# Kernel optimization log

Hardware: AMD Instinct MI355X
Metric: run time of the kernel (lower is better)

Reference implementation:

```python
import jax, jax.numpy as jnp
import numpy as np

B, S, H, L, O = 128, 2048, 128, 2, 2  # batch, seq, hidden(=input), layers, output


def setup_inputs() -> dict:
    key = jax.random.key(0)
    k1, k2, k3, k4, k5 = jax.random.split(key, 5)
    std = 1.0 / np.sqrt(H)
    x_data = jax.random.normal(k1, (B, S, H), dtype=jnp.float32)
    x_length = jax.random.randint(k2, (B,), 0, S, dtype=jnp.int32)
    x_label = jax.random.uniform(k3, (B,), dtype=jnp.float32)
    # torch Linear layout: y = x @ W.T ; init uniform(-1/sqrt(H), 1/sqrt(H))
    Wx2h = jax.random.uniform(k4, (L, 2 * H, H), minval=-std, maxval=std, dtype=jnp.float32)
    Wfc = jax.random.uniform(k5, (L, O, H), minval=-std, maxval=std, dtype=jnp.float32)
    return {"x_data": x_data, "x_length": x_length, "x_label": x_label,
            "Wx2h": Wx2h, "Wfc": Wfc}


def reference(x_data, x_length, x_label, Wx2h, Wfc):
    Bn, Sn, Hn = x_data.shape
    Ln = Wx2h.shape[0]
    # valid-timestep mask: seq index < x_length[i]
    mask = (jnp.arange(Sn)[None, :] < x_length[:, None]).astype(x_data.dtype)  # [B,S]

    def step(carry, inp):
        S1, S2 = carry            # each [L,B,H]
        x_t, m_t = inp            # [B,H], [B]
        h = x_t
        out = None
        S1_new, S2_new = [], []
        for l in range(Ln):
            gate = h @ Wx2h[l].T                    # [B,2H]
            m1, m2 = jnp.split(gate, 2, axis=1)
            s1n = S1[l] + jnp.tanh(m1)
            s2n = S2[l] + jnp.tanh(m2)
            Fu = jax.nn.relu(s1n)
            h = (1.0 - Fu) * s2n + Fu * S2[l]       # hy
            out = jax.nn.softmax(h @ Wfc[l].T, axis=1)  # [B,O]
            S1_new.append(s1n)
            S2_new.append(s2n)
        loss_t = m_t * (x_label - jax.nn.sigmoid(out[:, 1])) ** 2  # [B]
        return (jnp.stack(S1_new), jnp.stack(S2_new)), loss_t

    S0 = jnp.zeros((Ln, Bn, Hn), x_data.dtype)
    xs = (jnp.swapaxes(x_data, 0, 1), mask.T)  # time-major [S,B,H], [S,B]
    _, losses = jax.lax.scan(step, (S0, S0), xs)
    return jnp.sum(losses)
```

## Files before the change

### kernel.cpp

```cpp
#include <hip/hip_runtime.h>

typedef __bf16 bf16;
typedef __bf16 bf16x8 __attribute__((ext_vector_type(8)));
typedef float floatx4 __attribute__((ext_vector_type(4)));

#define BATCH 128
#define SEQ   2048
#define HID   128
#define TWOH  256
#define CH    128
#define NCH   16
#define MTOT  (BATCH * SEQ)

__device__ __forceinline__ float fast_tanh(float x) {
    float e = __builtin_amdgcn_exp2f(2.88539008177793f * x);
    return 1.0f - 2.0f * __builtin_amdgcn_rcpf(e + 1.0f);
}
__device__ __forceinline__ float fast_sigmoid(float x) {
    return __builtin_amdgcn_rcpf(1.0f + __builtin_amdgcn_exp2f(-1.44269504088896f * x));
}

union PK4 { unsigned long long u; bf16 h[4]; };
union PK8 { uint4 u; bf16 h[8]; };

__global__ __launch_bounds__(256) void convert_w_k(const float* __restrict__ W,
                                                   bf16* __restrict__ Wb) {
    int i = blockIdx.x * 256 + threadIdx.x;
    float4 v = ((const float4*)W)[i];
    PK4 pk;
    pk.h[0] = (bf16)v.x; pk.h[1] = (bf16)v.y;
    pk.h[2] = (bf16)v.z; pk.h[3] = (bf16)v.w;
    ((unsigned long long*)Wb)[i] = pk.u;
}

__device__ __forceinline__ void tile_prefix(const float g[4][4], float pref[4][4],
                                            float* stripe_tot, int quad, int l16) {
    float mibase = 0.f;
    #pragma unroll
    for (int mi = 0; mi < 4; ++mi) {
        float s0 = g[mi][0];
        float s1 = s0 + g[mi][1];
        float s2 = s1 + g[mi][2];
        float s3 = s2 + g[mi][3];
        float tot = s3, xq = tot;
        float t = __shfl_up(xq, 16);
        if (quad >= 1) xq += t;
        t = __shfl_up(xq, 32);
        if (quad >= 2) xq += t;
        float excl = mibase + xq - tot;
        pref[mi][0] = excl + s0;
        pref[mi][1] = excl + s1;
        pref[mi][2] = excl + s2;
        pref[mi][3] = excl + s3;
        mibase += __shfl(xq, 48 + l16);
    }
    *stripe_tot = mibase;
}

__device__ __forceinline__ void load_wf(const bf16* __restrict__ Wh, bf16x8 wf[4][2],
                                        int wc, int quad, int l16) {
    #pragma unroll
    for (int s = 0; s < 4; ++s)
        #pragma unroll
        for (int ni = 0; ni < 2; ++ni) {
            int n = wc * 32 + ni * 16 + l16;
            int kg = s * 4 + quad;
            wf[s][ni] = *(const bf16x8*)&Wh[n * 128 + kg * 8];
        }
}

__device__ __forceinline__ void gemm_tile(const bf16* As, const bf16x8 wf[4][2],
                                          floatx4 acc[4][2], int wr, int quad, int l16) {
    #pragma unroll
    for (int s = 0; s < 4; ++s) {
        int kg = s * 4 + quad;
        bf16x8 af[4];
        #pragma unroll
        for (int mi = 0; mi < 4; ++mi) {
            int r = wr * 64 + mi * 16 + l16;
            af[mi] = *(const bf16x8*)&As[r * 128 + ((kg ^ (r & 7)) << 3)];
        }
        #pragma unroll
        for (int mi = 0; mi < 4; ++mi)
            #pragma unroll
            for (int ni = 0; ni < 2; ++ni)
                acc[mi][ni] = __builtin_amdgcn_mfma_f32_16x16x32_bf16(
                    af[mi], wf[s][ni], acc[mi][ni], 0, 0, 0);
    }
}


__global__ __launch_bounds__(512, 4) void l0_k(const float* __restrict__ x,
                                               const bf16* __restrict__ Wb,
                                               uint4* __restrict__ T,
                                               float* __restrict__ Pout) {
    __shared__ bf16 As[128 * 128];
    __shared__ float psum[512];

    const int tid  = threadIdx.x;
    const int lane = tid & 63;
    const int wid  = tid >> 6;
    const int wr   = wid >> 2;
    const int wc   = wid & 3;
    const int quad = lane >> 4;
    const int l16  = lane & 15;
    const long blk = blockIdx.x;
    const long rowBase = blk * 128;

    {
        const float4* A4 = (const float4*)(x + rowBase * HID);
        #pragma unroll
        for (int it = 0; it < 8; ++it) {
            int i  = it * 512 + tid;
            int r  = i >> 5;
            int c4 = i & 31;
            float4 v = A4[i];
            int g = c4 >> 1, hf = c4 & 1;
            PK4 pk;
            pk.h[0] = (bf16)v.x; pk.h[1] = (bf16)v.y;
            pk.h[2] = (bf16)v.z; pk.h[3] = (bf16)v.w;
            *(unsigned long long*)&As[r * 128 + ((g ^ (r & 7)) << 3) + (hf << 2)] = pk.u;
        }
    }

    bf16x8 wf[4][2];
    load_wf(Wb, wf, wc, quad, l16);
    __syncthreads();

    #pragma unroll
    for (int half = 0; half < 2; ++half) {
        floatx4 acc[4][2];
        #pragma unroll
        for (int a = 0; a < 4; ++a)
            #pragma unroll
            for (int b2 = 0; b2 < 2; ++b2) acc[a][b2] = (floatx4){0.f, 0.f, 0.f, 0.f};

        gemm_tile(As, wf, acc, wr, quad, l16);
        if (half == 0)
            load_wf(Wb + (size_t)128 * HID, wf, wc, quad, l16);

        float g2[2][4][4];
        #pragma unroll
        for (int mi = 0; mi < 4; ++mi)
            #pragma unroll
            for (int ni = 0; ni < 2; ++ni)
                #pragma unroll
                for (int rr = 0; rr < 4; ++rr)
                    g2[ni][mi][rr] = fast_tanh(acc[mi][ni][rr]);

        #pragma unroll
        for (int mi = 0; mi < 4; ++mi) {
            PK8 p;
            #pragma unroll
            for (int rr = 0; rr < 4; ++rr) {
                p.h[rr]     = (bf16)g2[0][mi][rr];
                p.h[4 + rr] = (bf16)g2[1][mi][rr];
            }
            T[((blk * 2 + half) * 4 + mi) * 512 + tid] = p.u;
        }

        #pragma unroll
        for (int ni = 0; ni < 2; ++ni) {
            float cs = 0.f;
            #pragma unroll
            for (int mi = 0; mi < 4; ++mi)
                #pragma unroll
                for (int rr = 0; rr < 4; ++rr) cs += g2[ni][mi][rr];
            cs += __shfl_xor(cs, 16);
            cs += __shfl_xor(cs, 32);
            if (quad == 0)
                psum[wr * 256 + half * 128 + wc * 32 + ni * 16 + l16] = cs;
        }
    }

    __syncthreads();
    if (tid < 256) Pout[(blk << 8) + tid] = psum[tid] + psum[256 + tid];
}

__global__ __launch_bounds__(512, 4) void l1_k(const bf16* __restrict__ Wb1,
                                               uint4* __restrict__ T,
                                               const float* __restrict__ P0,
                                               float* __restrict__ Pout) {
    __shared__ bf16 As[128 * 128];
    __shared__ float offP[256];
    __shared__ float auxp[128];
    __shared__ float psum[512];

    const int tid  = threadIdx.x;
    const int lane = tid & 63;
    const int wid  = tid >> 6;
    const int wr   = wid >> 2;
    const int wc   = wid & 3;
    const int quad = lane >> 4;
    const int l16  = lane & 15;
    const long blk = blockIdx.x;
    const int  bb  = (int)(blk >> 4);
    const int  cc  = (int)(blk & 15);

    if (tid < 256) {
        float a = 0.f;
        for (int cp = 0; cp < cc; ++cp)
            a += P0[(((long)(bb * NCH + cp)) << 8) + tid];
        offP[tid] = a;
    }

    float p1[2][4][4];

    {
        float g2[2][4][4];
        #pragma unroll
        for (int mi = 0; mi < 4; ++mi) {
            PK8 p;
            p.u = T[((blk * 2 + 0) * 4 + mi) * 512 + tid];
            #pragma unroll
            for (int rr = 0; rr < 4; ++rr) {
                g2[0][mi][rr] = (float)p.h[rr];
                g2[1][mi][rr] = (float)p.h[4 + rr];
            }
        }
        float pref[2][4][4], st[2];
        #pragma unroll
        for (int ni = 0; ni < 2; ++ni) {
            tile_prefix(g2[ni], pref[ni], &st[ni], quad, l16);
            if (wr == 0 && quad == 0) auxp[wc * 32 + ni * 16 + l16] = st[ni];
        }
        __syncthreads();
        #pragma unroll
        for (int ni = 0; ni < 2; ++ni) {
            int col = wc * 32 + ni * 16 + l16;
            float off = offP[col];
            if (wr) off += auxp[col];
            #pragma unroll
            for (int mi = 0; mi < 4; ++mi)
                #pragma unroll
                for (int rr = 0; rr < 4; ++rr)
                    p1[ni][mi][rr] = pref[ni][mi][rr] + off;
        }
    }
    __syncthreads();

    {
        float g2[2][4][4];
        #pragma unroll
        for (int mi = 0; mi < 4; ++mi) {
            PK8 p;
            p.u = T[((blk * 2 + 1) * 4 + mi) * 512 + tid];
            #pragma unroll
            for (int rr = 0; rr < 4; ++rr) {
                g2[0][mi][rr] = (float)p.h[rr];
                g2[1][mi][rr] = (float)p.h[4 + rr];
            }
        }
        float pref[2][4][4], st[2];
        #pragma unroll
        for (int ni = 0; ni < 2; ++ni) {
            tile_prefix(g2[ni], pref[ni], &st[ni], quad, l16);
            if (wr == 0 && quad == 0) auxp[wc * 32 + ni * 16 + l16] = st[ni];
        }
        __syncthreads();
        #pragma unroll
        for (int ni = 0; ni < 2; ++ni) {
            int col = wc * 32 + ni * 16 + l16;
            int gsw = col >> 3, rem = col & 7;
            float off = offP[128 + col];
            if (wr) off += auxp[col];
            #pragma unroll
            for (int mi = 0; mi < 4; ++mi)
                #pragma unroll
                for (int rr = 0; rr < 4; ++rr) {
                    int row = wr * 64 + mi * 16 + quad * 4 + rr;
                    float h = pref[ni][mi][rr] + off -
                              fmaxf(p1[ni][mi][rr], 0.f) * g2[ni][mi][rr];
                    As[row * 128 + ((gsw ^ (row & 7)) << 3) + rem] = (bf16)h;
                }
        }
    }

    bf16x8 wf[4][2];
    load_wf(Wb1, wf, wc, quad, l16);
    __syncthreads();

    #pragma unroll
    for (int half = 0; half < 2; ++half) {
        floatx4 acc[4][2];
        #pragma unroll
        for (int a = 0; a < 4; ++a)
            #pragma unroll
            for (int b2 = 0; b2 < 2; ++b2) acc[a][b2] = (floatx4){0.f, 0.f, 0.f, 0.f};

        gemm_tile(As, wf, acc, wr, quad, l16);
        if (half == 0)
            load_wf(Wb1 + (size_t)128 * HID, wf, wc, quad, l16);

        float g2[2][4][4];
        #pragma unroll
        for (int mi = 0; mi < 4; ++mi)
            #pragma unroll
            for (int ni = 0; ni < 2; ++ni)
                #pragma unroll
                for (int rr = 0; rr < 4; ++rr)
                    g2[ni][mi][rr] = fast_tanh(acc[mi][ni][rr]);

        #pragma unroll
        for (int mi = 0; mi < 4; ++mi) {
            PK8 p;
            #pragma unroll
            for (int rr = 0; rr < 4; ++rr) {
                p.h[rr]     = (bf16)g2[0][mi][rr];
                p.h[4 + rr] = (bf16)g2[1][mi][rr];
            }
            T[((blk * 2 + half) * 4 + mi) * 512 + tid] = p.u;
        }

        #pragma unroll
        for (int ni = 0; ni < 2; ++ni) {
            float cs = 0.f;
            #pragma unroll
            for (int mi = 0; mi < 4; ++mi)
                #pragma unroll
                for (int rr = 0; rr < 4; ++rr) cs += g2[ni][mi][rr];
            cs += __shfl_xor(cs, 16);
            cs += __shfl_xor(cs, 32);
            if (quad == 0)
                psum[wr * 256 + half * 128 + wc * 32 + ni * 16 + l16] = cs;
        }
    }

    __syncthreads();
    if (tid < 256) Pout[(blk << 8) + tid] = psum[tid] + psum[256 + tid];
}

__global__ __launch_bounds__(512, 4) void loss_k(const uint4* __restrict__ T,
                                                 const float* __restrict__ P1,
                                                 const float* __restrict__ Wfc,
                                                 const int* __restrict__ xlen,
                                                 const float* __restrict__ xlab,
                                                 float* __restrict__ out) {
    __shared__ float offP[256];
    __shared__ float auxp[128];
    __shared__ float zbuf[4][128][2];
    __shared__ float red[2];

    const int tid  = threadIdx.x;
    const int lane = tid & 63;
    const int wid  = tid >> 6;
    const int wr   = wid >> 2;
    const int wc   = wid & 3;
    const int quad = lane >> 4;
    const int l16  = lane & 15;
    const long blk = blockIdx.x;
    const int  bb  = (int)(blk >> 4);
    const int  cc  = (int)(blk & 15);

    if (tid < 256) {
        float a = 0.f;
        for (int cp = 0; cp < cc; ++cp)
            a += P1[(((long)(bb * NCH + cp)) << 8) + tid];
        offP[tid] = a;
    }

    float p1[2][4][4];

    {
        float g2[2][4][4];
        #pragma unroll
        for (int mi = 0; mi < 4; ++mi) {
            PK8 p;
            p.u = T[((blk * 2 + 0) * 4 + mi) * 512 + tid];
            #pragma unroll
            for (int rr = 0; rr < 4; ++rr) {
                g2[0][mi][rr] = (float)p.h[rr];
                g2[1][mi][rr] = (float)p.h[4 + rr];
            }
        }
        float pref[2][4][4], st[2];
        #pragma unroll
        for (int ni = 0; ni < 2; ++ni) {
            tile_prefix(g2[ni], pref[ni], &st[ni], quad, l16);
            if (wr == 0 && quad == 0) auxp[wc * 32 + ni * 16 + l16] = st[ni];
        }
        __syncthreads();
        #pragma unroll
        for (int ni = 0; ni < 2; ++ni) {
            int col = wc * 32 + ni * 16 + l16;
            float off = offP[col];
            if (wr) off += auxp[col];
            #pragma unroll
            for (int mi = 0; mi < 4; ++mi)
                #pragma unroll
                for (int rr = 0; rr < 4; ++rr)
                    p1[ni][mi][rr] = pref[ni][mi][rr] + off;
        }
    }
    __syncthreads();

    {
        float g2[2][4][4];
        #pragma unroll
        for (int mi = 0; mi < 4; ++mi) {
            PK8 p;
            p.u = T[((blk * 2 + 1) * 4 + mi) * 512 + tid];
            #pragma unroll
            for (int rr = 0; rr < 4; ++rr) {
                g2[0][mi][rr] = (float)p.h[rr];
                g2[1][mi][rr] = (float)p.h[4 + rr];
            }
        }
        float pref[2][4][4], st[2];
        #pragma unroll
        for (int ni = 0; ni < 2; ++ni) {
            tile_prefix(g2[ni], pref[ni], &st[ni], quad, l16);
            if (wr == 0 && quad == 0) auxp[wc * 32 + ni * 16 + l16] = st[ni];
        }
        __syncthreads();

        float w0[2], w1[2], off[2];
        #pragma unroll
        for (int ni = 0; ni < 2; ++ni) {
            int col = wc * 32 + ni * 16 + l16;
            w0[ni] = Wfc[2 * HID + col];
            w1[ni] = Wfc[3 * HID + col];
            off[ni] = offP[128 + col];
            if (wr) off[ni] += auxp[col];
        }
        #pragma unroll
        for (int mi = 0; mi < 4; ++mi)
            #pragma unroll
            for (int rr = 0; rr < 4; ++rr) {
                float z0 = 0.f, z1 = 0.f;
                #pragma unroll
                for (int ni = 0; ni < 2; ++ni) {
                    float h = pref[ni][mi][rr] + off[ni] -
                              fmaxf(p1[ni][mi][rr], 0.f) * g2[ni][mi][rr];
                    z0 += h * w0[ni];
                    z1 += h * w1[ni];
                }
                z0 += __shfl_xor(z0, 1); z1 += __shfl_xor(z1, 1);
                z0 += __shfl_xor(z0, 2); z1 += __shfl_xor(z1, 2);
                z0 += __shfl_xor(z0, 4); z1 += __shfl_xor(z1, 4);
                z0 += __shfl_xor(z0, 8); z1 += __shfl_xor(z1, 8);
                if (l16 == 0) {
                    int row = wr * 64 + mi * 16 + quad * 4 + rr;
                    zbuf[wc][row][0] = z0;
                    zbuf[wc][row][1] = z1;
                }
            }
    }

    __syncthreads();
    float lsum = 0.f;
    if (tid < 128) {
        int row = tid;
        float z0 = zbuf[0][row][0] + zbuf[1][row][0] + zbuf[2][row][0] + zbuf[3][row][0];
        float z1 = zbuf[0][row][1] + zbuf[1][row][1] + zbuf[2][row][1] + zbuf[3][row][1];
        float o1 = fast_sigmoid(z1 - z0);
        float sg = fast_sigmoid(o1);
        float d = xlab[bb] - sg;
        if (cc * CH + row < xlen[bb]) lsum = d * d;
        lsum += __shfl_xor(lsum, 1);
        lsum += __shfl_xor(lsum, 2);
        lsum += __shfl_xor(lsum, 4);
        lsum += __shfl_xor(lsum, 8);
        lsum += __shfl_xor(lsum, 16);
        lsum += __shfl_xor(lsum, 32);
        if (lane == 0) red[wid] = lsum;
    }
    __syncthreads();
    if (tid == 0) atomicAdd(out, red[0] + red[1]);
}

extern "C" void kernel_launch(void* const* d_in, const int* in_sizes, int n_in,
                              void* d_out, int out_size, void* d_ws, size_t ws_size,
                              hipStream_t stream) {
    const float* x    = (const float*)d_in[0];
    const int*   xlen = (const int*)d_in[1];
    const float* xlab = (const float*)d_in[2];
    const float* Wx2h = (const float*)d_in[3];
    const float* Wfc  = (const float*)d_in[4];
    float* out = (float*)d_out;

    char* ws = (char*)d_ws;
    uint4* T  = (uint4*)ws;
    float* P0 = (float*)(ws + (size_t)MTOT * TWOH * 2);
    float* P1 = P0 + (size_t)BATCH * NCH * TWOH;
    bf16*  Wb = (bf16*)(P1 + (size_t)BATCH * NCH * TWOH);

    hipMemsetAsync(d_out, 0, sizeof(float), stream);
    convert_w_k<<<64, 256, 0, stream>>>(Wx2h, Wb);

    l0_k<<<MTOT / 128, 512, 0, stream>>>(x, Wb, T, P0);
    l1_k<<<MTOT / 128, 512, 0, stream>>>(Wb + (size_t)TWOH * HID, T, P0, P1);
    loss_k<<<MTOT / 128, 512, 0, stream>>>(T, P1, Wfc, xlen, xlab, out);
}
```

Baseline: 366.3 us.

## Skip fully masked sequence chunks and stage swizzled weights in shared memory

```diff
diff --git a/kernel.cpp b/kernel.cpp
--- a/kernel.cpp
+++ b/kernel.cpp
@@ -27,10 +27,15 @@
                                                    bf16* __restrict__ Wb) {
     int i = blockIdx.x * 256 + threadIdx.x;
     float4 v = ((const float4*)W)[i];
+    int R  = i >> 5;
+    int k0 = (i & 31) << 2;
+    int n  = R & 127;
+    int g  = k0 >> 3;
+    int j0 = k0 & 7;
     PK4 pk;
     pk.h[0] = (bf16)v.x; pk.h[1] = (bf16)v.y;
     pk.h[2] = (bf16)v.z; pk.h[3] = (bf16)v.w;
-    ((unsigned long long*)Wb)[i] = pk.u;
+    *(unsigned long long*)&Wb[R * 128 + ((g ^ (n & 7)) << 3) + j0] = pk.u;
 }
 
 __device__ __forceinline__ void tile_prefix(const float g[4][4], float pref[4][4],
@@ -57,44 +62,68 @@
     *stripe_tot = mibase;
 }
 
-__device__ __forceinline__ void load_wf(const bf16* __restrict__ Wh, bf16x8 wf[4][2],
-                                        int wc, int quad, int l16) {
-    #pragma unroll
-    for (int s = 0; s < 4; ++s)
-        #pragma unroll
-        for (int ni = 0; ni < 2; ++ni) {
-            int n = wc * 32 + ni * 16 + l16;
-            int kg = s * 4 + quad;
-            wf[s][ni] = *(const bf16x8*)&Wh[n * 128 + kg * 8];
-        }
-}
-
-__device__ __forceinline__ void gemm_tile(const bf16* As, const bf16x8 wf[4][2],
-                                          floatx4 acc[4][2], int wr, int quad, int l16) {
+__device__ __forceinline__ void gemm_tile(const bf16* As, const bf16* Bs,
+                                          floatx4 acc[4][2], int wr, int wc,
+                                          int quad, int l16) {
     #pragma unroll
     for (int s = 0; s < 4; ++s) {
         int kg = s * 4 + quad;
-        bf16x8 af[4];
+        bf16x8 af[4], bfr[2];
         #pragma unroll
         for (int mi = 0; mi < 4; ++mi) {
             int r = wr * 64 + mi * 16 + l16;
             af[mi] = *(const bf16x8*)&As[r * 128 + ((kg ^ (r & 7)) << 3)];
         }
         #pragma unroll
+        for (int ni = 0; ni < 2; ++ni) {
+            int n = wc * 32 + ni * 16 + l16;
+            bfr[ni] = *(const bf16x8*)&Bs[n * 128 + ((kg ^ (n & 7)) << 3)];
+        }
+        #pragma unroll
         for (int mi = 0; mi < 4; ++mi)
             #pragma unroll
             for (int ni = 0; ni < 2; ++ni)
                 acc[mi][ni] = __builtin_amdgcn_mfma_f32_16x16x32_bf16(
-                    af[mi], wf[s][ni], acc[mi][ni], 0, 0, 0);
+                    af[mi], bfr[ni], acc[mi][ni], 0, 0, 0);
+    }
+}
+
+__device__ __forceinline__ void load_T_half(const uint4* __restrict__ T, long blk,
+                                            int half, int tid, float g2[2][4][4]) {
+    #pragma unroll
+    for (int mi = 0; mi < 4; ++mi) {
+        PK8 p;
+        p.u = T[((blk * 2 + half) * 4 + mi) * 512 + tid];
+        #pragma unroll
+        for (int rr = 0; rr < 4; ++rr) {
+            g2[0][mi][rr] = (float)p.h[rr];
+            g2[1][mi][rr] = (float)p.h[4 + rr];
+        }
+    }
+}
+
+__device__ __forceinline__ void store_T_half(uint4* __restrict__ T, long blk,
+                                             int half, int tid, const float g2[2][4][4]) {
+    #pragma unroll
+    for (int mi = 0; mi < 4; ++mi) {
+        PK8 p;
+        #pragma unroll
+        for (int rr = 0; rr < 4; ++rr) {
+            p.h[rr]     = (bf16)g2[0][mi][rr];
+            p.h[4 + rr] = (bf16)g2[1][mi][rr];
+        }
+        T[((blk * 2 + half) * 4 + mi) * 512 + tid] = p.u;
     }
 }
 
 
 __global__ __launch_bounds__(512, 4) void l0_k(const float* __restrict__ x,
-                                               const bf16* __restrict__ Wb,
+                                               const bf16* __restrict__ Wbs,
                                                uint4* __restrict__ T,
-                                               float* __restrict__ Pout) {
+                                               float* __restrict__ Pout,
+                                               const int* __restrict__ xlen) {
     __shared__ bf16 As[128 * 128];
+    __shared__ bf16 Bs[128 * 128];
     __shared__ float psum[512];
 
     const int tid  = threadIdx.x;
@@ -105,7 +134,18 @@
     const int quad = lane >> 4;
     const int l16  = lane & 15;
     const long blk = blockIdx.x;
+    const int  bb  = (int)(blk >> 4);
+    const int  cc  = (int)(blk & 15);
+    if ((cc << 7) >= xlen[bb]) return;
+
     const long rowBase = blk * 128;
+
+    uint4 wv[4];
+    {
+        const uint4* W8 = (const uint4*)Wbs;
+        #pragma unroll
+        for (int it = 0; it < 4; ++it) wv[it] = W8[it * 512 + tid];
+    }
 
     {
         const float4* A4 = (const float4*)(x + rowBase * HID);
@@ -123,8 +163,15 @@
         }
     }
 
-    bf16x8 wf[4][2];
-    load_wf(Wb, wf, wc, quad, l16);
+    #pragma unroll
+    for (int it = 0; it < 4; ++it)
+        *(uint4*)&Bs[(it * 512 + tid) * 8] = wv[it];
+
+    {
+        const uint4* W8 = (const uint4*)(Wbs + 128 * HID);
+        #pragma unroll
+        for (int it = 0; it < 4; ++it) wv[it] = W8[it * 512 + tid];
+    }
     __syncthreads();
 
     #pragma unroll
@@ -135,9 +182,14 @@
             #pragma unroll
             for (int b2 = 0; b2 < 2; ++b2) acc[a][b2] = (floatx4){0.f, 0.f, 0.f, 0.f};
 
-        gemm_tile(As, wf, acc, wr, quad, l16);
-        if (half == 0)
-            load_wf(Wb + (size_t)128 * HID, wf, wc, quad, l16);
+        gemm_tile(As, Bs, acc, wr, wc, quad, l16);
+
+        if (half == 0) {
+            __syncthreads();
+            #pragma unroll
+            for (int it = 0; it < 4; ++it)
+                *(uint4*)&Bs[(it * 512 + tid) * 8] = wv[it];
+        }
 
         float g2[2][4][4];
         #pragma unroll
@@ -148,16 +200,7 @@
                 for (int rr = 0; rr < 4; ++rr)
                     g2[ni][mi][rr] = fast_tanh(acc[mi][ni][rr]);
 
-        #pragma unroll
-        for (int mi = 0; mi < 4; ++mi) {
-            PK8 p;
-            #pragma unroll
-            for (int rr = 0; rr < 4; ++rr) {
-                p.h[rr]     = (bf16)g2[0][mi][rr];
-                p.h[4 + rr] = (bf16)g2[1][mi][rr];
-            }
-            T[((blk * 2 + half) * 4 + mi) * 512 + tid] = p.u;
-        }
+        store_T_half(T, blk, half, tid, g2);
 
         #pragma unroll
         for (int ni = 0; ni < 2; ++ni) {
@@ -171,17 +214,21 @@
             if (quad == 0)
                 psum[wr * 256 + half * 128 + wc * 32 + ni * 16 + l16] = cs;
         }
+
+        if (half == 0) __syncthreads();
     }
 
     __syncthreads();
     if (tid < 256) Pout[(blk << 8) + tid] = psum[tid] + psum[256 + tid];
 }
 
-__global__ __launch_bounds__(512, 4) void l1_k(const bf16* __restrict__ Wb1,
+__global__ __launch_bounds__(512, 4) void l1_k(const bf16* __restrict__ Wb1s,
                                                uint4* __restrict__ T,
                                                const float* __restrict__ P0,
-                                               float* __restrict__ Pout) {
+                                               float* __restrict__ Pout,
+                                               const int* __restrict__ xlen) {
     __shared__ bf16 As[128 * 128];
+    __shared__ bf16 Bs[128 * 128];
     __shared__ float offP[256];
     __shared__ float auxp[128];
     __shared__ float psum[512];
@@ -196,33 +243,43 @@
     const long blk = blockIdx.x;
     const int  bb  = (int)(blk >> 4);
     const int  cc  = (int)(blk & 15);
-
+    if ((cc << 7) >= xlen[bb]) return;
+
+    uint4 wv[4];
+    {
+        const uint4* W8 = (const uint4*)Wb1s;
+        #pragma unroll
+        for (int it = 0; it < 4; ++it) wv[it] = W8[it * 512 + tid];
+    }
+
+    float pv = 0.f;
     if (tid < 256) {
-        float a = 0.f;
-        for (int cp = 0; cp < cc; ++cp)
-            a += P0[(((long)(bb * NCH + cp)) << 8) + tid];
-        offP[tid] = a;
+        #pragma unroll
+        for (int cp = 0; cp < NCH - 1; ++cp) {
+            float v = P0[(((long)(bb * NCH + cp)) << 8) + tid];
+            pv += (cp < cc) ? v : 0.f;
+        }
     }
 
     float p1[2][4][4];
 
     {
         float g2[2][4][4];
-        #pragma unroll
-        for (int mi = 0; mi < 4; ++mi) {
-            PK8 p;
-            p.u = T[((blk * 2 + 0) * 4 + mi) * 512 + tid];
-            #pragma unroll
-            for (int rr = 0; rr < 4; ++rr) {
-                g2[0][mi][rr] = (float)p.h[rr];
-                g2[1][mi][rr] = (float)p.h[4 + rr];
-            }
-        }
+        load_T_half(T, blk, 0, tid, g2);
+        if (tid < 256) offP[tid] = pv;
         float pref[2][4][4], st[2];
         #pragma unroll
         for (int ni = 0; ni < 2; ++ni) {
             tile_prefix(g2[ni], pref[ni], &st[ni], quad, l16);
             if (wr == 0 && quad == 0) auxp[wc * 32 + ni * 16 + l16] = st[ni];
+        }
+        #pragma unroll
+        for (int it = 0; it < 4; ++it)
+            *(uint4*)&Bs[(it * 512 + tid) * 8] = wv[it];
+        {
+            const uint4* W8 = (const uint4*)(Wb1s + 128 * HID);
+            #pragma unroll
+            for (int it = 0; it < 4; ++it) wv[it] = W8[it * 512 + tid];
         }
         __syncthreads();
         #pragma unroll
@@ -241,16 +298,7 @@
 
     {
         float g2[2][4][4];
-        #pragma unroll
-        for (int mi = 0; mi < 4; ++mi) {
-            PK8 p;
-            p.u = T[((blk * 2 + 1) * 4 + mi) * 512 + tid];
-            #pragma unroll
-            for (int rr = 0; rr < 4; ++rr) {
-                g2[0][mi][rr] = (float)p.h[rr];
-                g2[1][mi][rr] = (float)p.h[4 + rr];
-            }
-        }
+        load_T_half(T, blk, 1, tid, g2);
         float pref[2][4][4], st[2];
         #pragma unroll
         for (int ni = 0; ni < 2; ++ni) {
@@ -275,9 +323,6 @@
                 }
         }
     }
-
-    bf16x8 wf[4][2];
-    load_wf(Wb1, wf, wc, quad, l16);
     __syncthreads();
 
     #pragma unroll
@@ -288,9 +333,14 @@
             #pragma unroll
             for (int b2 = 0; b2 < 2; ++b2) acc[a][b2] = (floatx4){0.f, 0.f, 0.f, 0.f};
 
-        gemm_tile(As, wf, acc, wr, quad, l16);
-        if (half == 0)
-            load_wf(Wb1 + (size_t)128 * HID, wf, wc, quad, l16);
+        gemm_tile(As, Bs, acc, wr, wc, quad, l16);
+
+        if (half == 0) {
+            __syncthreads();
+            #pragma unroll
+            for (int it = 0; it < 4; ++it)
+                *(uint4*)&Bs[(it * 512 + tid) * 8] = wv[it];
+        }
 
         float g2[2][4][4];
         #pragma unroll
@@ -301,16 +351,7 @@
                 for (int rr = 0; rr < 4; ++rr)
                     g2[ni][mi][rr] = fast_tanh(acc[mi][ni][rr]);
 
-        #pragma unroll
-        for (int mi = 0; mi < 4; ++mi) {
-            PK8 p;
-            #pragma unroll
-            for (int rr = 0; rr < 4; ++rr) {
-                p.h[rr]     = (bf16)g2[0][mi][rr];
-                p.h[4 + rr] = (bf16)g2[1][mi][rr];
-            }
-            T[((blk * 2 + half) * 4 + mi) * 512 + tid] = p.u;
-        }
+        store_T_half(T, blk, half, tid, g2);
 
         #pragma unroll
         for (int ni = 0; ni < 2; ++ni) {
@@ -324,6 +365,8 @@
             if (quad == 0)
                 psum[wr * 256 + half * 128 + wc * 32 + ni * 16 + l16] = cs;
         }
+
+        if (half == 0) __syncthreads();
     }
 
     __syncthreads();
@@ -351,28 +394,23 @@
     const long blk = blockIdx.x;
     const int  bb  = (int)(blk >> 4);
     const int  cc  = (int)(blk & 15);
-
+    if ((cc << 7) >= xlen[bb]) return;
+
+    float pv = 0.f;
     if (tid < 256) {
-        float a = 0.f;
-        for (int cp = 0; cp < cc; ++cp)
-            a += P1[(((long)(bb * NCH + cp)) << 8) + tid];
-        offP[tid] = a;
+        #pragma unroll
+        for (int cp = 0; cp < NCH - 1; ++cp) {
+            float v = P1[(((long)(bb * NCH + cp)) << 8) + tid];
+            pv += (cp < cc) ? v : 0.f;
+        }
     }
 
     float p1[2][4][4];
 
     {
         float g2[2][4][4];
-        #pragma unroll
-        for (int mi = 0; mi < 4; ++mi) {
-            PK8 p;
-            p.u = T[((blk * 2 + 0) * 4 + mi) * 512 + tid];
-            #pragma unroll
-            for (int rr = 0; rr < 4; ++rr) {
-                g2[0][mi][rr] = (float)p.h[rr];
-                g2[1][mi][rr] = (float)p.h[4 + rr];
-            }
-        }
+        load_T_half(T, blk, 0, tid, g2);
+        if (tid < 256) offP[tid] = pv;
         float pref[2][4][4], st[2];
         #pragma unroll
         for (int ni = 0; ni < 2; ++ni) {
@@ -396,16 +434,7 @@
 
     {
         float g2[2][4][4];
-        #pragma unroll
-        for (int mi = 0; mi < 4; ++mi) {
-            PK8 p;
-            p.u = T[((blk * 2 + 1) * 4 + mi) * 512 + tid];
-            #pragma unroll
-            for (int rr = 0; rr < 4; ++rr) {
-                g2[0][mi][rr] = (float)p.h[rr];
-                g2[1][mi][rr] = (float)p.h[4 + rr];
-            }
-        }
+        load_T_half(T, blk, 1, tid, g2);
         float pref[2][4][4], st[2];
         #pragma unroll
         for (int ni = 0; ni < 2; ++ni) {
@@ -488,7 +517,7 @@
     hipMemsetAsync(d_out, 0, sizeof(float), stream);
     convert_w_k<<<64, 256, 0, stream>>>(Wx2h, Wb);
 
-    l0_k<<<MTOT / 128, 512, 0, stream>>>(x, Wb, T, P0);
-    l1_k<<<MTOT / 128, 512, 0, stream>>>(Wb + (size_t)TWOH * HID, T, P0, P1);
+    l0_k<<<MTOT / 128, 512, 0, stream>>>(x, Wb, T, P0, xlen);
+    l1_k<<<MTOT / 128, 512, 0, stream>>>(Wb + (size_t)TWOH * HID, T, P0, P1, xlen);
     loss_k<<<MTOT / 128, 512, 0, stream>>>(T, P1, Wfc, xlen, xlab, out);
 }
```

After: 355.5 us. 1.03x faster.
